# Performance work log

Hardware: AMD Instinct MI355X
Metric: run time of the kernel (lower is better)

## Reference

```python
import jax, jax.numpy as jnp
import numpy as np

N_NODES = 50000
NEG_SLOPE = 0.2  # PyG GATConv default


def setup_inputs() -> dict:
    key = jax.random.key(0)
    ks = jax.random.split(key, 10)
    N, D_IN, HID, H, D_OUT, E = N_NODES, 256, 64, 4, 40, 800000
    inp = {
        "x": jax.random.normal(ks[0], (N, D_IN), jnp.float32),
        "edge_index": jax.random.randint(ks[1], (2, E), 0, N, jnp.int32),
        "W1": jax.random.normal(ks[2], (D_IN, H * HID), jnp.float32) * (1.0 / np.sqrt(D_IN)),
        "att_src1": jax.random.normal(ks[3], (H, HID), jnp.float32) * 0.1,
        "att_dst1": jax.random.normal(ks[4], (H, HID), jnp.float32) * 0.1,
        "b1": jnp.zeros((H * HID,), jnp.float32),
        "W2": jax.random.normal(ks[5], (H * HID, D_OUT), jnp.float32) * (1.0 / np.sqrt(H * HID)),
        "att_src2": jax.random.normal(ks[6], (1, D_OUT), jnp.float32) * 0.1,
        "att_dst2": jax.random.normal(ks[7], (1, D_OUT), jnp.float32) * 0.1,
        "b2": jnp.zeros((D_OUT,), jnp.float32),
    }
    return inp


def _gat_conv(x, src, dst, W, a_src, a_dst, b, n_nodes):
    """One GATConv layer (PyG semantics, self-loops already in src/dst)."""
    H, F = a_src.shape
    h = (x @ W).reshape(n_nodes, H, F)                      # [N,H,F]
    a_s = jnp.einsum('nhf,hf->nh', h, a_src)                # [N,H]
    a_d = jnp.einsum('nhf,hf->nh', h, a_dst)                # [N,H]
    e = jax.nn.leaky_relu(a_s[src] + a_d[dst], NEG_SLOPE)   # [E,H]
    # segment softmax over incoming edges of each destination node
    m = jax.ops.segment_max(e, dst, num_segments=n_nodes)   # [N,H]
    ex = jnp.exp(e - m[dst])                                # [E,H]
    den = jax.ops.segment_sum(ex, dst, num_segments=n_nodes)
    alpha = ex / den[dst]                                   # [E,H]
    out = jax.ops.segment_sum(h[src] * alpha[:, :, None], dst, num_segments=n_nodes)
    return out.reshape(n_nodes, H * F) + b


def reference(x, edge_index, W1, att_src1, att_dst1, b1, W2, att_src2, att_dst2, b2):
    N = x.shape[0]
    loop = jnp.arange(N, dtype=edge_index.dtype)
    src = jnp.concatenate([edge_index[0], loop])
    dst = jnp.concatenate([edge_index[1], loop])
    h = jax.nn.relu(_gat_conv(x, src, dst, W1, att_src1, att_dst1, b1, N))
    logits = _gat_conv(h, src, dst, W2, att_src2, att_dst2, b2, N)
    return jax.nn.log_softmax(logits, axis=1)
```

## Files before the change

kernel.cpp:

```cpp
#include <hip/hip_runtime.h>
#include <hip/hip_fp16.h>
#include <math.h>

#define NEG_SLOPE 0.2f

typedef short short8v __attribute__((ext_vector_type(8)));
typedef _Float16 half8v __attribute__((ext_vector_type(8)));
typedef float f32x4 __attribute__((ext_vector_type(4)));

__device__ __forceinline__ unsigned short f2bf(float f) {
    unsigned int u = __builtin_bit_cast(unsigned int, f);
    u += 0x7FFFu + ((u >> 16) & 1u);
    return (unsigned short)(u >> 16);
}

__device__ __forceinline__ void fma_h4(float4& acc, float w, uint2 v) {
    __half2 p0 = __builtin_bit_cast(__half2, v.x);
    __half2 p1 = __builtin_bit_cast(__half2, v.y);
    float2 f0 = __half22float2(p0), f1 = __half22float2(p1);
    acc.x += w * f0.x; acc.y += w * f0.y; acc.z += w * f1.x; acc.w += w * f1.y;
}

__global__ void k_deg_cvt(const int* __restrict__ ei, int E, int N, int degB,
                          int* __restrict__ deg, int* __restrict__ rank,
                          const float* __restrict__ W1, const float* __restrict__ W2,
                          unsigned short* __restrict__ w1t, __half* __restrict__ w2t) {
    int b = blockIdx.x;
    if (b < degB) {
        int i = b * 256 + threadIdx.x;
        int Et = E + N;
        if (i >= Et) return;
        int dst = (i < E) ? ei[E + i] : (i - E);
        rank[i] = atomicAdd(&deg[dst], 1);
    } else {
        int bb = b - degB;
        int k = threadIdx.x;
        if (bb < 256) {
            w1t[bb * 256 + k] = f2bf(W1[k * 256 + bb]);
        } else {
            int c = bb - 256;
            w2t[c * 256 + k] = __float2half((c < 40) ? W2[k * 40 + c] : 0.f);
        }
    }
}

__global__ void k_scan_block(const int* __restrict__ deg, int N, int* __restrict__ excl, int* __restrict__ bsums) {
    __shared__ int s[256];
    int b = blockIdx.x, t = threadIdx.x;
    int i = b * 256 + t;
    int v = (i < N) ? deg[i] : 0;
    s[t] = v;
    __syncthreads();
    for (int off = 1; off < 256; off <<= 1) {
        int add = (t >= off) ? s[t - off] : 0;
        __syncthreads();
        s[t] += add;
        __syncthreads();
    }
    int incl = s[t];
    if (i < N) excl[i] = incl - v;
    if (t == 255) bsums[b] = incl;
}

__global__ void k_scan_add(int* __restrict__ row_start, const int* __restrict__ bsums,
                           int N, int Et, int NB) {
    __shared__ int ws[4];
    int b = blockIdx.x, t = threadIdx.x;
    int wv = t >> 6, l = t & 63;
    int v = (t < b && t < NB) ? bsums[t] : 0;
    for (int off = 32; off; off >>= 1) v += __shfl_xor(v, off);
    if (l == 0) ws[wv] = v;
    __syncthreads();
    int total = ws[0] + ws[1] + ws[2] + ws[3];
    int i = b * 256 + t;
    if (i < N) row_start[i] += total;
    if (i == 0) row_start[N] = Et;
}

__global__ void k_scatter(const int* __restrict__ ei, const int* __restrict__ rank, int E, int N,
                          const int* __restrict__ row_start, int* __restrict__ csr_src) {
    int i = blockIdx.x * blockDim.x + threadIdx.x;
    int Et = E + N;
    if (i >= Et) return;
    int src, dst;
    if (i < E) { src = ei[i]; dst = ei[E + i]; }
    else       { src = i - E; dst = i - E; }
    csr_src[row_start[dst] + rank[i]] = src;
}

#define LDP 264
__global__ __launch_bounds__(256) void k_gemm1_mfma(const float* __restrict__ x,
                                                    const unsigned short* __restrict__ w1t,
                                                    const float* __restrict__ att_s,
                                                    const float* __restrict__ att_d,
                                                    __half* __restrict__ h1h,
                                                    float* __restrict__ as1, float* __restrict__ ad1, int N) {
    __shared__ unsigned short As[64 * LDP];
    __shared__ unsigned short Bs[64 * LDP];
    int tid = threadIdx.x;
    int row0 = blockIdx.x * 64;
#pragma unroll
    for (int it = 0; it < 16; it++) {
        int c = tid + it * 256;
        int r = c >> 6, q = c & 63;
        float4 v = make_float4(0, 0, 0, 0);
        if (row0 + r < N) v = ((const float4*)x)[(size_t)(row0 + r) * 64 + q];
        ushort4 o;
        o.x = f2bf(v.x); o.y = f2bf(v.y); o.z = f2bf(v.z); o.w = f2bf(v.w);
        *(ushort4*)&As[r * LDP + q * 4] = o;
    }
    int w = tid >> 6, l = tid & 63;
    int hi = l >> 4, lo = l & 15;
    short8v a[8];
    for (int head = 0; head < 4; head++) {
#pragma unroll
        for (int it = 0; it < 8; it++) {
            int c = tid + it * 256;
            int r = c >> 5, q = c & 31;
            uint4 vb = ((const uint4*)w1t)[(size_t)(head * 64 + r) * 32 + q];
            *(uint4*)&Bs[r * LDP + q * 8] = vb;
        }
        __syncthreads();
        if (head == 0) {
#pragma unroll
            for (int kk = 0; kk < 8; kk++)
                a[kk] = *(const short8v*)&As[(16 * w + lo) * LDP + kk * 32 + 8 * hi];
        }
        f32x4 acc[4] = {};
#pragma unroll
        for (int kk = 0; kk < 8; kk++) {
#pragma unroll
            for (int jb = 0; jb < 4; jb++) {
                short8v b = *(const short8v*)&Bs[(16 * jb + lo) * LDP + kk * 32 + 8 * hi];
                acc[jb] = __builtin_amdgcn_mfma_f32_16x16x32_bf16(a[kk], b, acc[jb], 0, 0, 0);
            }
        }
        float asr[4], adr[4];
#pragma unroll
        for (int jb = 0; jb < 4; jb++) {
            int c = head * 64 + lo + 16 * jb;
            asr[jb] = att_s[c];
            adr[jb] = att_d[c];
        }
#pragma unroll
        for (int j = 0; j < 4; j++) {
            int rr = 16 * w + 4 * hi + j;
            int r = row0 + rr;
            float s = 0.f, d = 0.f;
#pragma unroll
            for (int jb = 0; jb < 4; jb++) {
                float v = acc[jb][j];
                s += v * asr[jb];
                d += v * adr[jb];
                if (r < N) h1h[(size_t)r * 256 + head * 64 + lo + 16 * jb] = __float2half(v);
            }
            s += __shfl_xor(s, 1); s += __shfl_xor(s, 2); s += __shfl_xor(s, 4); s += __shfl_xor(s, 8);
            d += __shfl_xor(d, 1); d += __shfl_xor(d, 2); d += __shfl_xor(d, 4); d += __shfl_xor(d, 8);
            if (lo == 0 && r < N) {
                as1[r * 4 + head] = s;
                ad1[r * 4 + head] = d;
            }
        }
        if (head < 3) __syncthreads();
    }
}

__global__ __launch_bounds__(256) void k_agg1(const __half* __restrict__ h1h, const float* __restrict__ as1,
                                              const float* __restrict__ ad1, const int* __restrict__ row_start,
                                              const int* __restrict__ csr_src, const float* __restrict__ b1,
                                              __half* __restrict__ hbh, int N) {
    __shared__ int    s_src[4][64];
    __shared__ float4 s_w[4][64];
    int wv = threadIdx.x >> 6, l = threadIdx.x & 63;
    int n = blockIdx.x * 4 + wv;
    if (n >= N) return;
    int s0 = row_start[n], s1 = row_start[n + 1];
    int head = l >> 4;
    unsigned lb8 = (unsigned)l * 8u;
    const char* h1b = (const char*)h1h;
    float4 adv = ((const float4*)ad1)[n];
    float4 acc0 = make_float4(0, 0, 0, 0), acc1 = acc0, acc2 = acc0, acc3 = acc0;
    float den = 0.f;
    for (int c0 = s0; c0 < s1; c0 += 64) {
        int cl = min(64, s1 - c0);
        if (l < cl) {
            int si = csr_src[c0 + l];
            s_src[wv][l] = si;
            float4 a = ((const float4*)as1)[si];
            float4 e;
            e.x = a.x + adv.x; e.x = e.x > 0.f ? e.x : NEG_SLOPE * e.x; e.x = __expf(e.x);
            e.y = a.y + adv.y; e.y = e.y > 0.f ? e.y : NEG_SLOPE * e.y; e.y = __expf(e.y);
            e.z = a.z + adv.z; e.z = e.z > 0.f ? e.z : NEG_SLOPE * e.z; e.z = __expf(e.z);
            e.w = a.w + adv.w; e.w = e.w > 0.f ? e.w : NEG_SLOPE * e.w; e.w = __expf(e.w);
            s_w[wv][l] = e;
        }
        int p = 0;
        for (; p + 8 <= cl; p += 8) {
            int ss[8]; float ww[8]; uint2 vv[8];
#pragma unroll
            for (int i = 0; i < 8; i++) {
                ss[i] = s_src[wv][p + i];
                ww[i] = ((const float*)&s_w[wv][p + i])[head];
            }
#pragma unroll
            for (int i = 0; i < 8; i++)
                vv[i] = *(const uint2*)(h1b + (unsigned)ss[i] * 512u + lb8);
#pragma unroll
            for (int i = 0; i < 8; i++) {
                den += ww[i];
                if ((i & 3) == 0) fma_h4(acc0, ww[i], vv[i]);
                if ((i & 3) == 1) fma_h4(acc1, ww[i], vv[i]);
                if ((i & 3) == 2) fma_h4(acc2, ww[i], vv[i]);
                if ((i & 3) == 3) fma_h4(acc3, ww[i], vv[i]);
            }
        }
        for (; p + 4 <= cl; p += 4) {
            int sA = s_src[wv][p],     sB = s_src[wv][p + 1];
            int sC = s_src[wv][p + 2], sD = s_src[wv][p + 3];
            float wA = ((const float*)&s_w[wv][p    ])[head];
            float wB = ((const float*)&s_w[wv][p + 1])[head];
            float wC = ((const float*)&s_w[wv][p + 2])[head];
            float wD = ((const float*)&s_w[wv][p + 3])[head];
            uint2 vA = *(const uint2*)(h1b + (unsigned)sA * 512u + lb8);
            uint2 vB = *(const uint2*)(h1b + (unsigned)sB * 512u + lb8);
            uint2 vC = *(const uint2*)(h1b + (unsigned)sC * 512u + lb8);
            uint2 vD = *(const uint2*)(h1b + (unsigned)sD * 512u + lb8);
            den += (wA + wB) + (wC + wD);
            fma_h4(acc0, wA, vA); fma_h4(acc1, wB, vB);
            fma_h4(acc2, wC, vC); fma_h4(acc3, wD, vD);
        }
        for (; p < cl; p++) {
            int s = s_src[wv][p];
            float wg = ((const float*)&s_w[wv][p])[head];
            uint2 v = *(const uint2*)(h1b + (unsigned)s * 512u + lb8);
            den += wg;
            fma_h4(acc0, wg, v);
        }
    }
    float4 acc;
    acc.x = (acc0.x + acc1.x) + (acc2.x + acc3.x);
    acc.y = (acc0.y + acc1.y) + (acc2.y + acc3.y);
    acc.z = (acc0.z + acc1.z) + (acc2.z + acc3.z);
    acc.w = (acc0.w + acc1.w) + (acc2.w + acc3.w);
    float inv = 1.f / den;
    float4 b = ((const float4*)b1)[l];
    float r0 = acc.x * inv + b.x; r0 = r0 > 0.f ? r0 : 0.f;
    float r1 = acc.y * inv + b.y; r1 = r1 > 0.f ? r1 : 0.f;
    float r2 = acc.z * inv + b.z; r2 = r2 > 0.f ? r2 : 0.f;
    float r3 = acc.w * inv + b.w; r3 = r3 > 0.f ? r3 : 0.f;
    unsigned short u0 = __builtin_bit_cast(unsigned short, __float2half(r0));
    unsigned short u1 = __builtin_bit_cast(unsigned short, __float2half(r1));
    unsigned short u2 = __builtin_bit_cast(unsigned short, __float2half(r2));
    unsigned short u3 = __builtin_bit_cast(unsigned short, __float2half(r3));
    uint2 st;
    st.x = (unsigned)u0 | ((unsigned)u1 << 16);
    st.y = (unsigned)u2 | ((unsigned)u3 << 16);
    *(uint2*)((char*)hbh + (unsigned)n * 512u + lb8) = st;
}

__global__ __launch_bounds__(256) void k_gemm2_mfma(const _Float16* __restrict__ hbh,
                                                    const _Float16* __restrict__ w2t,
                                                    const float* __restrict__ att_s2,
                                                    const float* __restrict__ att_d2,
                                                    __half* __restrict__ h2h,
                                                    float* __restrict__ as2, float* __restrict__ ad2, int N) {
    __shared__ _Float16 Hs[64 * LDP];
    __shared__ _Float16 Ws[48 * LDP];
    int tid = threadIdx.x;
    int row0 = blockIdx.x * 64;
#pragma unroll
    for (int it = 0; it < 8; it++) {
        int c = tid + it * 256;
        int r = c >> 5, q = c & 31;
        uint4 v = make_uint4(0, 0, 0, 0);
        if (row0 + r < N) v = ((const uint4*)hbh)[(size_t)(row0 + r) * 32 + q];
        *(uint4*)&Hs[r * LDP + q * 8] = v;
    }
#pragma unroll
    for (int it = 0; it < 6; it++) {
        int c = tid + it * 256;
        int r = c >> 5, q = c & 31;
        uint4 v = ((const uint4*)w2t)[c];
        *(uint4*)&Ws[r * LDP + q * 8] = v;
    }
    __syncthreads();
    int w = tid >> 6, l = tid & 63;
    int hi = l >> 4, lo = l & 15;
    f32x4 acc[3] = {};
#pragma unroll
    for (int kk = 0; kk < 8; kk++) {
        half8v a = *(const half8v*)&Hs[(16 * w + lo) * LDP + kk * 32 + 8 * hi];
#pragma unroll
        for (int jb = 0; jb < 3; jb++) {
            half8v b = *(const half8v*)&Ws[(16 * jb + lo) * LDP + kk * 32 + 8 * hi];
            acc[jb] = __builtin_amdgcn_mfma_f32_16x16x32_f16(a, b, acc[jb], 0, 0, 0);
        }
    }
    float asr[3], adr[3];
#pragma unroll
    for (int jb = 0; jb < 3; jb++) {
        int c = 16 * jb + lo;
        asr[jb] = (c < 40) ? att_s2[c] : 0.f;
        adr[jb] = (c < 40) ? att_d2[c] : 0.f;
    }
#pragma unroll
    for (int j = 0; j < 4; j++) {
        int r = row0 + 16 * w + 4 * hi + j;
        float s = 0.f, d = 0.f;
#pragma unroll
        for (int jb = 0; jb < 3; jb++) {
            float v = acc[jb][j];
            s += v * asr[jb];
            d += v * adr[jb];
            int c = 16 * jb + lo;
            if (c < 40 && r < N) h2h[(size_t)r * 40 + c] = __float2half(v);
        }
        s += __shfl_xor(s, 1); s += __shfl_xor(s, 2); s += __shfl_xor(s, 4); s += __shfl_xor(s, 8);
        d += __shfl_xor(d, 1); d += __shfl_xor(d, 2); d += __shfl_xor(d, 4); d += __shfl_xor(d, 8);
        if (lo == 0 && r < N) { as2[r] = s; ad2[r] = d; }
    }
}

__global__ __launch_bounds__(256) void k_agg2(const __half* __restrict__ h2h, const float* __restrict__ as2,
                                              const float* __restrict__ ad2, const int* __restrict__ row_start,
                                              const int* __restrict__ csr_src, const float* __restrict__ b2,
                                              float* __restrict__ out, int N) {
    __shared__ int   s_src[4][64];
    __shared__ float s_w[4][64];
    int wv = threadIdx.x >> 6, l = threadIdx.x & 63;
    int n = blockIdx.x * 4 + wv;
    if (n >= N) return;
    int s0 = row_start[n], s1 = row_start[n + 1];
    int grp = l / 20, li = l - grp * 20;
    unsigned li4 = (unsigned)li * 4u;
    const char* h2b = (const char*)h2h;
    float ad = ad2[n];
    float2 accA = make_float2(0.f, 0.f), accB = accA;
    float denA = 0.f, denB = 0.f;
    bool act = grp < 3;
    for (int c0 = s0; c0 < s1; c0 += 64) {
        int cl = min(64, s1 - c0);
        if (l < cl) {
            int si = csr_src[c0 + l];
            s_src[wv][l] = si;
            float e = as2[si] + ad;
            e = e > 0.f ? e : NEG_SLOPE * e;
            s_w[wv][l] = __expf(e);
        }
        if (act) {
            int p = grp;
            for (; p + 3 < cl; p += 6) {
                int sA = s_src[wv][p], sB = s_src[wv][p + 3];
                float wA = s_w[wv][p], wB = s_w[wv][p + 3];
                unsigned vA = *(const unsigned*)(h2b + (unsigned)sA * 80u + li4);
                unsigned vB = *(const unsigned*)(h2b + (unsigned)sB * 80u + li4);
                denA += wA; denB += wB;
                float2 fA = __half22float2(__builtin_bit_cast(__half2, vA));
                float2 fB = __half22float2(__builtin_bit_cast(__half2, vB));
                accA.x += wA * fA.x; accA.y += wA * fA.y;
                accB.x += wB * fB.x; accB.y += wB * fB.y;
            }
            for (; p < cl; p += 3) {
                int si = s_src[wv][p];
                float w = s_w[wv][p];
                unsigned v = *(const unsigned*)(h2b + (unsigned)si * 80u + li4);
                denA += w;
                float2 f = __half22float2(__builtin_bit_cast(__half2, v));
                accA.x += w * f.x; accA.y += w * f.y;
            }
        }
    }
    float den = denA + denB;
    float2 acc = make_float2(accA.x + accB.x, accA.y + accB.y);
    float den_t = __shfl(den, li) + __shfl(den, 20 + li) + __shfl(den, 40 + li);
    float ax = acc.x + __shfl(acc.x, l + 20) + __shfl(acc.x, l + 40);
    float ay = acc.y + __shfl(acc.y, l + 20) + __shfl(acc.y, l + 40);
    float inv = 1.f / den_t;
    float lg0 = -1e30f, lg1 = -1e30f;
    if (l < 20) {
        lg0 = ax * inv + b2[2 * l];
        lg1 = ay * inv + b2[2 * l + 1];
    }
    float mx = fmaxf(lg0, lg1);
    for (int off = 32; off; off >>= 1) mx = fmaxf(mx, __shfl_xor(mx, off));
    float s = (l < 20) ? (__expf(lg0 - mx) + __expf(lg1 - mx)) : 0.f;
    for (int off = 32; off; off >>= 1) s += __shfl_xor(s, off);
    float ls = logf(s);
    if (l < 20) {
        out[(size_t)n * 40 + 2 * l]     = lg0 - mx - ls;
        out[(size_t)n * 40 + 2 * l + 1] = lg1 - mx - ls;
    }
}

extern "C" void kernel_launch(void* const* d_in, const int* in_sizes, int n_in,
                              void* d_out, int out_size, void* d_ws, size_t ws_size,
                              hipStream_t stream) {
    const float* x      = (const float*)d_in[0];
    const int*   ei     = (const int*)d_in[1];
    const float* W1     = (const float*)d_in[2];
    const float* att_s1 = (const float*)d_in[3];
    const float* att_d1 = (const float*)d_in[4];
    const float* b1     = (const float*)d_in[5];
    const float* W2     = (const float*)d_in[6];
    const float* att_s2 = (const float*)d_in[7];
    const float* att_d2 = (const float*)d_in[8];
    const float* b2     = (const float*)d_in[9];

    int N = in_sizes[0] / 256;
    int E = in_sizes[1] / 2;
    int Et = E + N;

    char* ws = (char*)d_ws;
    size_t off = 0;
    auto alloc = [&](size_t bytes) -> void* {
        void* p = ws + off;
        off += (bytes + 255) / 256 * 256;
        return p;
    };
    __half* h1h = (__half*)alloc((size_t)N * 256 * 2);
    __half* hbh = (__half*)alloc((size_t)N * 256 * 2);
    __half* h2h = (__half*)alloc((size_t)N * 40 * 2);
    unsigned short* w1t = (unsigned short*)alloc((size_t)256 * 256 * 2);
    __half* w2t = (__half*)alloc((size_t)48 * 256 * 2);
    float* as1 = (float*)alloc((size_t)N * 4 * 4);
    float* ad1 = (float*)alloc((size_t)N * 4 * 4);
    float* as2 = (float*)alloc((size_t)N * 4);
    float* ad2 = (float*)alloc((size_t)N * 4);
    int* deg       = (int*)alloc((size_t)N * 4);
    int* rank      = (int*)alloc((size_t)Et * 4);
    int* row_start = (int*)alloc((size_t)(N + 1) * 4);
    int* csr_src   = (int*)alloc((size_t)Et * 4);
    int NB = (N + 255) / 256;
    int* bsums = (int*)alloc((size_t)NB * 4);

    hipMemsetAsync(deg, 0, (size_t)N * 4, stream);

    int degB = (Et + 255) / 256;
    k_deg_cvt<<<degB + 304, 256, 0, stream>>>(ei, E, N, degB, deg, rank, W1, W2, w1t, w2t);
    k_scan_block<<<NB, 256, 0, stream>>>(deg, N, row_start, bsums);
    k_scan_add<<<NB, 256, 0, stream>>>(row_start, bsums, N, Et, NB);
    k_scatter<<<(Et + 255) / 256, 256, 0, stream>>>(ei, rank, E, N, row_start, csr_src);

    k_gemm1_mfma<<<(N + 63) / 64, 256, 0, stream>>>(x, w1t, att_s1, att_d1, h1h, as1, ad1, N);
    k_agg1<<<(N + 3) / 4, 256, 0, stream>>>(h1h, as1, ad1, row_start, csr_src, b1, hbh, N);
    k_gemm2_mfma<<<(N + 63) / 64, 256, 0, stream>>>((const _Float16*)hbh, (const _Float16*)w2t,
                                                    att_s2, att_d2, h2h, as2, ad2, N);
    k_agg2<<<(N + 3) / 4, 256, 0, stream>>>(h2h, as2, ad2, row_start, csr_src, b2, (float*)d_out, N);
}
```

Before: 202.6 us.

## Fuse CSR scatter into GEMM1 launch and double-buffer W1 tiles in LDS

The CSR scatter kernel is merged into the layer-1 GEMM kernel as extra blocks, so the two independent jobs share one launch and can run at the same time. Inside the GEMM, the W1 tile for the next head is loaded into registers while the current head's MFMAs run, then written to the alternate LDS buffer (As is reused once the A fragments sit in registers). This is meant to remove one launch and hide the global load latency of the weights. In exchange it adds register pressure and makes the scatter blocks occupy GEMM-sized LDS allocations.

```diff
diff --git a/kernel.cpp b/kernel.cpp
--- a/kernel.cpp
+++ b/kernel.cpp
@@ -77,27 +77,30 @@
     if (i == 0) row_start[N] = Et;
 }
 
-__global__ void k_scatter(const int* __restrict__ ei, const int* __restrict__ rank, int E, int N,
-                          const int* __restrict__ row_start, int* __restrict__ csr_src) {
-    int i = blockIdx.x * blockDim.x + threadIdx.x;
-    int Et = E + N;
-    if (i >= Et) return;
-    int src, dst;
-    if (i < E) { src = ei[i]; dst = ei[E + i]; }
-    else       { src = i - E; dst = i - E; }
-    csr_src[row_start[dst] + rank[i]] = src;
-}
-
 #define LDP 264
-__global__ __launch_bounds__(256) void k_gemm1_mfma(const float* __restrict__ x,
-                                                    const unsigned short* __restrict__ w1t,
-                                                    const float* __restrict__ att_s,
-                                                    const float* __restrict__ att_d,
-                                                    __half* __restrict__ h1h,
-                                                    float* __restrict__ as1, float* __restrict__ ad1, int N) {
+__global__ __launch_bounds__(256) void k_gemm1_sc(const float* __restrict__ x,
+                                                  const unsigned short* __restrict__ w1t,
+                                                  const float* __restrict__ att_s,
+                                                  const float* __restrict__ att_d,
+                                                  __half* __restrict__ h1h,
+                                                  float* __restrict__ as1, float* __restrict__ ad1, int N,
+                                                  const int* __restrict__ ei, const int* __restrict__ rank,
+                                                  const int* __restrict__ row_start, int* __restrict__ csr_src,
+                                                  int E, int gemmB) {
     __shared__ unsigned short As[64 * LDP];
     __shared__ unsigned short Bs[64 * LDP];
     int tid = threadIdx.x;
+    if (blockIdx.x >= gemmB) {
+        int i = (blockIdx.x - gemmB) * 256 + tid;
+        int Et = E + N;
+        if (i < Et) {
+            int src, dst;
+            if (i < E) { src = ei[i]; dst = ei[E + i]; }
+            else       { src = i - E; dst = i - E; }
+            csr_src[row_start[dst] + rank[i]] = src;
+        }
+        return;
+    }
     int row0 = blockIdx.x * 64;
 #pragma unroll
     for (int it = 0; it < 16; it++) {
@@ -109,29 +112,40 @@
         o.x = f2bf(v.x); o.y = f2bf(v.y); o.z = f2bf(v.z); o.w = f2bf(v.w);
         *(ushort4*)&As[r * LDP + q * 4] = o;
     }
+    {
+        uint4 vb[8];
+#pragma unroll
+        for (int it = 0; it < 8; it++) vb[it] = ((const uint4*)w1t)[tid + it * 256];
+#pragma unroll
+        for (int it = 0; it < 8; it++) {
+            int c = tid + it * 256;
+            int r = c >> 5, q = c & 31;
+            *(uint4*)&Bs[r * LDP + q * 8] = vb[it];
+        }
+    }
+    __syncthreads();
     int w = tid >> 6, l = tid & 63;
     int hi = l >> 4, lo = l & 15;
     short8v a[8];
+#pragma unroll
+    for (int kk = 0; kk < 8; kk++)
+        a[kk] = *(const short8v*)&As[(16 * w + lo) * LDP + kk * 32 + 8 * hi];
+    __syncthreads();
     for (int head = 0; head < 4; head++) {
-#pragma unroll
-        for (int it = 0; it < 8; it++) {
-            int c = tid + it * 256;
-            int r = c >> 5, q = c & 31;
-            uint4 vb = ((const uint4*)w1t)[(size_t)(head * 64 + r) * 32 + q];
-            *(uint4*)&Bs[r * LDP + q * 8] = vb;
-        }
-        __syncthreads();
-        if (head == 0) {
-#pragma unroll
-            for (int kk = 0; kk < 8; kk++)
-                a[kk] = *(const short8v*)&As[(16 * w + lo) * LDP + kk * 32 + 8 * hi];
+        unsigned short* cur = (head & 1) ? As : Bs;
+        unsigned short* nxt = (head & 1) ? Bs : As;
+        uint4 vb[8];
+        if (head < 3) {
+#pragma unroll
+            for (int it = 0; it < 8; it++)
+                vb[it] = ((const uint4*)w1t)[(head + 1) * 2048 + tid + it * 256];
         }
         f32x4 acc[4] = {};
 #pragma unroll
         for (int kk = 0; kk < 8; kk++) {
 #pragma unroll
             for (int jb = 0; jb < 4; jb++) {
-                short8v b = *(const short8v*)&Bs[(16 * jb + lo) * LDP + kk * 32 + 8 * hi];
+                short8v b = *(const short8v*)&cur[(16 * jb + lo) * LDP + kk * 32 + 8 * hi];
                 acc[jb] = __builtin_amdgcn_mfma_f32_16x16x32_bf16(a[kk], b, acc[jb], 0, 0, 0);
             }
         }
@@ -161,7 +175,15 @@
                 ad1[r * 4 + head] = d;
             }
         }
-        if (head < 3) __syncthreads();
+        if (head < 3) {
+#pragma unroll
+            for (int it = 0; it < 8; it++) {
+                int c = tid + it * 256;
+                int r = c >> 5, q = c & 31;
+                *(uint4*)&nxt[r * LDP + q * 8] = vb[it];
+            }
+            __syncthreads();
+        }
     }
 }
 
@@ -439,9 +461,10 @@
     k_deg_cvt<<<degB + 304, 256, 0, stream>>>(ei, E, N, degB, deg, rank, W1, W2, w1t, w2t);
     k_scan_block<<<NB, 256, 0, stream>>>(deg, N, row_start, bsums);
     k_scan_add<<<NB, 256, 0, stream>>>(row_start, bsums, N, Et, NB);
-    k_scatter<<<(Et + 255) / 256, 256, 0, stream>>>(ei, rank, E, N, row_start, csr_src);
-
-    k_gemm1_mfma<<<(N + 63) / 64, 256, 0, stream>>>(x, w1t, att_s1, att_d1, h1h, as1, ad1, N);
+
+    int gemmB = (N + 63) / 64;
+    k_gemm1_sc<<<gemmB + degB, 256, 0, stream>>>(x, w1t, att_s1, att_d1, h1h, as1, ad1, N,
+                                                 ei, rank, row_start, csr_src, E, gemmB);
     k_agg1<<<(N + 3) / 4, 256, 0, stream>>>(h1h, as1, ad1, row_start, csr_src, b1, hbh, N);
     k_gemm2_mfma<<<(N + 63) / 64, 256, 0, stream>>>((const _Float16*)hbh, (const _Float16*)w2t,
                                                     att_s2, att_d2, h2h, as2, ad2, N);
```

Result: slower. 208.4 us (+2.9%).

## Slice layer-1 features into 32-column planes and split aggregation per slice

Applied to the files above, without the earlier changes.

Stores h1 and the aggregated hidden features as 8 column-slices of 32 halfs (64 B per node per slice) instead of 512 B rows. The layer-1 aggregation launches 8 blocks per node group, one per slice, and each wave processes 8 edges at a time with 8 lanes per edge, then reduces with cross-lane shuffles. The aim is to shrink the gathered working set per kernel pass so that feature gathers hit cache better and more edges are in flight per wave. In exchange, each edge's attention weight is recomputed 8 times, the GEMM1 stores and GEMM2 loads become strided, and csr_src/as1 are read once per slice.

```diff
diff --git a/kernel.cpp b/kernel.cpp
--- a/kernel.cpp
+++ b/kernel.cpp
@@ -93,7 +93,7 @@
                                                     const unsigned short* __restrict__ w1t,
                                                     const float* __restrict__ att_s,
                                                     const float* __restrict__ att_d,
-                                                    __half* __restrict__ h1h,
+                                                    __half* __restrict__ h1s,
                                                     float* __restrict__ as1, float* __restrict__ ad1, int N) {
     __shared__ unsigned short As[64 * LDP];
     __shared__ unsigned short Bs[64 * LDP];
@@ -152,7 +152,10 @@
                 float v = acc[jb][j];
                 s += v * asr[jb];
                 d += v * adr[jb];
-                if (r < N) h1h[(size_t)r * 256 + head * 64 + lo + 16 * jb] = __float2half(v);
+                if (r < N) {
+                    int c = head * 64 + lo + 16 * jb;
+                    h1s[((size_t)(c >> 5) * N + r) * 32 + (c & 31)] = __float2half(v);
+                }
             }
             s += __shfl_xor(s, 1); s += __shfl_xor(s, 2); s += __shfl_xor(s, 4); s += __shfl_xor(s, 8);
             d += __shfl_xor(d, 1); d += __shfl_xor(d, 2); d += __shfl_xor(d, 4); d += __shfl_xor(d, 8);
@@ -165,100 +168,69 @@
     }
 }
 
-__global__ __launch_bounds__(256) void k_agg1(const __half* __restrict__ h1h, const float* __restrict__ as1,
+__global__ __launch_bounds__(256) void k_agg1(const __half* __restrict__ h1s, const float* __restrict__ as1,
                                               const float* __restrict__ ad1, const int* __restrict__ row_start,
                                               const int* __restrict__ csr_src, const float* __restrict__ b1,
-                                              __half* __restrict__ hbh, int N) {
-    __shared__ int    s_src[4][64];
-    __shared__ float4 s_w[4][64];
+                                              __half* __restrict__ hbs, int N) {
     int wv = threadIdx.x >> 6, l = threadIdx.x & 63;
-    int n = blockIdx.x * 4 + wv;
+    int slice = blockIdx.x & 7;
+    int n = (blockIdx.x >> 3) * 4 + wv;
     if (n >= N) return;
+    int head = slice >> 1;
+    int g = l >> 3, k = l & 7;
     int s0 = row_start[n], s1 = row_start[n + 1];
-    int head = l >> 4;
-    unsigned lb8 = (unsigned)l * 8u;
-    const char* h1b = (const char*)h1h;
-    float4 adv = ((const float4*)ad1)[n];
-    float4 acc0 = make_float4(0, 0, 0, 0), acc1 = acc0, acc2 = acc0, acc3 = acc0;
-    float den = 0.f;
-    for (int c0 = s0; c0 < s1; c0 += 64) {
-        int cl = min(64, s1 - c0);
-        if (l < cl) {
-            int si = csr_src[c0 + l];
-            s_src[wv][l] = si;
-            float4 a = ((const float4*)as1)[si];
-            float4 e;
-            e.x = a.x + adv.x; e.x = e.x > 0.f ? e.x : NEG_SLOPE * e.x; e.x = __expf(e.x);
-            e.y = a.y + adv.y; e.y = e.y > 0.f ? e.y : NEG_SLOPE * e.y; e.y = __expf(e.y);
-            e.z = a.z + adv.z; e.z = e.z > 0.f ? e.z : NEG_SLOPE * e.z; e.z = __expf(e.z);
-            e.w = a.w + adv.w; e.w = e.w > 0.f ? e.w : NEG_SLOPE * e.w; e.w = __expf(e.w);
-            s_w[wv][l] = e;
-        }
-        int p = 0;
-        for (; p + 8 <= cl; p += 8) {
-            int ss[8]; float ww[8]; uint2 vv[8];
-#pragma unroll
-            for (int i = 0; i < 8; i++) {
-                ss[i] = s_src[wv][p + i];
-                ww[i] = ((const float*)&s_w[wv][p + i])[head];
-            }
-#pragma unroll
-            for (int i = 0; i < 8; i++)
-                vv[i] = *(const uint2*)(h1b + (unsigned)ss[i] * 512u + lb8);
-#pragma unroll
-            for (int i = 0; i < 8; i++) {
-                den += ww[i];
-                if ((i & 3) == 0) fma_h4(acc0, ww[i], vv[i]);
-                if ((i & 3) == 1) fma_h4(acc1, ww[i], vv[i]);
-                if ((i & 3) == 2) fma_h4(acc2, ww[i], vv[i]);
-                if ((i & 3) == 3) fma_h4(acc3, ww[i], vv[i]);
-            }
-        }
-        for (; p + 4 <= cl; p += 4) {
-            int sA = s_src[wv][p],     sB = s_src[wv][p + 1];
-            int sC = s_src[wv][p + 2], sD = s_src[wv][p + 3];
-            float wA = ((const float*)&s_w[wv][p    ])[head];
-            float wB = ((const float*)&s_w[wv][p + 1])[head];
-            float wC = ((const float*)&s_w[wv][p + 2])[head];
-            float wD = ((const float*)&s_w[wv][p + 3])[head];
-            uint2 vA = *(const uint2*)(h1b + (unsigned)sA * 512u + lb8);
-            uint2 vB = *(const uint2*)(h1b + (unsigned)sB * 512u + lb8);
-            uint2 vC = *(const uint2*)(h1b + (unsigned)sC * 512u + lb8);
-            uint2 vD = *(const uint2*)(h1b + (unsigned)sD * 512u + lb8);
-            den += (wA + wB) + (wC + wD);
-            fma_h4(acc0, wA, vA); fma_h4(acc1, wB, vB);
-            fma_h4(acc2, wC, vC); fma_h4(acc3, wD, vD);
-        }
-        for (; p < cl; p++) {
-            int s = s_src[wv][p];
-            float wg = ((const float*)&s_w[wv][p])[head];
-            uint2 v = *(const uint2*)(h1b + (unsigned)s * 512u + lb8);
-            den += wg;
-            fma_h4(acc0, wg, v);
-        }
+    float adv = ad1[n * 4 + head];
+    const char* hb = (const char*)h1s + (size_t)slice * N * 64u;
+    float4 accA = make_float4(0, 0, 0, 0), accB = accA;
+    float denA = 0.f, denB = 0.f;
+    for (int c0 = s0; c0 < s1; c0 += 16) {
+        int pA = c0 + g, pB = c0 + 8 + g;
+        bool okA = pA < s1, okB = pB < s1;
+        int sA = okA ? csr_src[pA] : 0;
+        int sB = okB ? csr_src[pB] : 0;
+        uint2 vA = make_uint2(0, 0), vB = make_uint2(0, 0);
+        float aA = 0.f, aB = 0.f;
+        if (okA) { aA = as1[sA * 4 + head]; vA = *(const uint2*)(hb + (unsigned)sA * 64u + (unsigned)k * 8u); }
+        if (okB) { aB = as1[sB * 4 + head]; vB = *(const uint2*)(hb + (unsigned)sB * 64u + (unsigned)k * 8u); }
+        float eA = aA + adv; eA = eA > 0.f ? eA : NEG_SLOPE * eA;
+        float eB = aB + adv; eB = eB > 0.f ? eB : NEG_SLOPE * eB;
+        float wA = okA ? __expf(eA) : 0.f;
+        float wB = okB ? __expf(eB) : 0.f;
+        denA += wA; denB += wB;
+        fma_h4(accA, wA, vA);
+        fma_h4(accB, wB, vB);
     }
     float4 acc;
-    acc.x = (acc0.x + acc1.x) + (acc2.x + acc3.x);
-    acc.y = (acc0.y + acc1.y) + (acc2.y + acc3.y);
-    acc.z = (acc0.z + acc1.z) + (acc2.z + acc3.z);
-    acc.w = (acc0.w + acc1.w) + (acc2.w + acc3.w);
+    acc.x = accA.x + accB.x; acc.y = accA.y + accB.y;
+    acc.z = accA.z + accB.z; acc.w = accA.w + accB.w;
+    float den = denA + denB;
+#pragma unroll
+    for (int m = 8; m <= 32; m <<= 1) {
+        acc.x += __shfl_xor(acc.x, m);
+        acc.y += __shfl_xor(acc.y, m);
+        acc.z += __shfl_xor(acc.z, m);
+        acc.w += __shfl_xor(acc.w, m);
+        den   += __shfl_xor(den, m);
+    }
     float inv = 1.f / den;
-    float4 b = ((const float4*)b1)[l];
+    float4 b = ((const float4*)b1)[slice * 8 + k];
     float r0 = acc.x * inv + b.x; r0 = r0 > 0.f ? r0 : 0.f;
     float r1 = acc.y * inv + b.y; r1 = r1 > 0.f ? r1 : 0.f;
     float r2 = acc.z * inv + b.z; r2 = r2 > 0.f ? r2 : 0.f;
     float r3 = acc.w * inv + b.w; r3 = r3 > 0.f ? r3 : 0.f;
-    unsigned short u0 = __builtin_bit_cast(unsigned short, __float2half(r0));
-    unsigned short u1 = __builtin_bit_cast(unsigned short, __float2half(r1));
-    unsigned short u2 = __builtin_bit_cast(unsigned short, __float2half(r2));
-    unsigned short u3 = __builtin_bit_cast(unsigned short, __float2half(r3));
-    uint2 st;
-    st.x = (unsigned)u0 | ((unsigned)u1 << 16);
-    st.y = (unsigned)u2 | ((unsigned)u3 << 16);
-    *(uint2*)((char*)hbh + (unsigned)n * 512u + lb8) = st;
-}
-
-__global__ __launch_bounds__(256) void k_gemm2_mfma(const _Float16* __restrict__ hbh,
+    if (g == 0) {
+        unsigned short u0 = __builtin_bit_cast(unsigned short, __float2half(r0));
+        unsigned short u1 = __builtin_bit_cast(unsigned short, __float2half(r1));
+        unsigned short u2 = __builtin_bit_cast(unsigned short, __float2half(r2));
+        unsigned short u3 = __builtin_bit_cast(unsigned short, __float2half(r3));
+        uint2 st;
+        st.x = (unsigned)u0 | ((unsigned)u1 << 16);
+        st.y = (unsigned)u2 | ((unsigned)u3 << 16);
+        *(uint2*)((char*)hbs + (size_t)slice * N * 64u + (unsigned)n * 64u + (unsigned)k * 8u) = st;
+    }
+}
+
+__global__ __launch_bounds__(256) void k_gemm2_mfma(const _Float16* __restrict__ hbs,
                                                     const _Float16* __restrict__ w2t,
                                                     const float* __restrict__ att_s2,
                                                     const float* __restrict__ att_d2,
@@ -272,8 +244,9 @@
     for (int it = 0; it < 8; it++) {
         int c = tid + it * 256;
         int r = c >> 5, q = c & 31;
+        int slice = q >> 2, off = q & 3;
         uint4 v = make_uint4(0, 0, 0, 0);
-        if (row0 + r < N) v = ((const uint4*)hbh)[(size_t)(row0 + r) * 32 + q];
+        if (row0 + r < N) v = ((const uint4*)hbs)[((size_t)slice * N + (row0 + r)) * 4 + off];
         *(uint4*)&Hs[r * LDP + q * 8] = v;
     }
 #pragma unroll
@@ -417,8 +390,8 @@
         off += (bytes + 255) / 256 * 256;
         return p;
     };
-    __half* h1h = (__half*)alloc((size_t)N * 256 * 2);
-    __half* hbh = (__half*)alloc((size_t)N * 256 * 2);
+    __half* h1s = (__half*)alloc((size_t)N * 256 * 2);
+    __half* hbs = (__half*)alloc((size_t)N * 256 * 2);
     __half* h2h = (__half*)alloc((size_t)N * 40 * 2);
     unsigned short* w1t = (unsigned short*)alloc((size_t)256 * 256 * 2);
     __half* w2t = (__half*)alloc((size_t)48 * 256 * 2);
@@ -439,11 +412,11 @@
     k_deg_cvt<<<degB + 304, 256, 0, stream>>>(ei, E, N, degB, deg, rank, W1, W2, w1t, w2t);
     k_scan_block<<<NB, 256, 0, stream>>>(deg, N, row_start, bsums);
     k_scan_add<<<NB, 256, 0, stream>>>(row_start, bsums, N, Et, NB);
-    k_scatter<<<(Et + 255) / 256, 256, 0, stream>>>(ei, rank, E, N, row_start, csr_src);
-
-    k_gemm1_mfma<<<(N + 63) / 64, 256, 0, stream>>>(x, w1t, att_s1, att_d1, h1h, as1, ad1, N);
-    k_agg1<<<(N + 3) / 4, 256, 0, stream>>>(h1h, as1, ad1, row_start, csr_src, b1, hbh, N);
-    k_gemm2_mfma<<<(N + 63) / 64, 256, 0, stream>>>((const _Float16*)hbh, (const _Float16*)w2t,
+    k_scatter<<<degB, 256, 0, stream>>>(ei, rank, E, N, row_start, csr_src);
+
+    k_gemm1_mfma<<<(N + 63) / 64, 256, 0, stream>>>(x, w1t, att_s1, att_d1, h1s, as1, ad1, N);
+    k_agg1<<<((N + 3) / 4) * 8, 256, 0, stream>>>(h1s, as1, ad1, row_start, csr_src, b1, hbs, N);
+    k_gemm2_mfma<<<(N + 63) / 64, 256, 0, stream>>>((const _Float16*)hbs, (const _Float16*)w2t,
                                                     att_s2, att_d2, h2h, as2, ad2, N);
     k_agg2<<<(N + 3) / 4, 256, 0, stream>>>(h2h, as2, ad2, row_start, csr_src, b2, (float*)d_out, N);
 }
```

Result: slower. 286.3 us (+41.4%).
